# Kernel tuning notes

Hardware: AMD Instinct MI355X
Metric: run time of the kernel (lower is better)

The kernel has to match this reference:

```python
import jax, jax.numpy as jnp
import numpy as np


def _lstm_layer(x, W_ih, W_hh, b_ih, b_hh):
    # x: [B, T, D]; W_ih: [4H, D]; W_hh: [4H, H]; gate order (PyTorch): i, f, g, o
    B, T, _ = x.shape
    H = W_hh.shape[1]
    # Precompute input contributions for all timesteps: [B, T, 4H]
    xg = jnp.einsum('btd,gd->btg', x, W_ih) + b_ih + b_hh

    def step(carry, xg_t):
        h, c = carry
        gates = xg_t + h @ W_hh.T  # [B, 4H]
        i, f, g, o = jnp.split(gates, 4, axis=-1)
        i = jax.nn.sigmoid(i)
        f = jax.nn.sigmoid(f)
        g = jnp.tanh(g)
        o = jax.nn.sigmoid(o)
        c = f * c + i * g
        h = o * jnp.tanh(c)
        return (h, c), h

    h0 = jnp.zeros((B, H), dtype=x.dtype)
    c0 = jnp.zeros((B, H), dtype=x.dtype)
    (_, _), hs = jax.lax.scan(step, (h0, c0), jnp.swapaxes(xg, 0, 1))
    return jnp.swapaxes(hs, 0, 1)  # [B, T, H]


def setup_inputs() -> dict:
    key = jax.random.key(0)
    ks = jax.random.split(key, 11)
    B, T, D, H, C = 262144, 8, 8, 16, 10
    s = 1.0 / np.sqrt(H)  # PyTorch LSTM init scale
    return {
        'input_data': jax.random.normal(ks[0], (B, T, D), dtype=jnp.float32),
        'W_ih_l0': jax.random.uniform(ks[1], (4 * H, D), jnp.float32, -s, s),
        'W_hh_l0': jax.random.uniform(ks[2], (4 * H, H), jnp.float32, -s, s),
        'b_ih_l0': jax.random.uniform(ks[3], (4 * H,), jnp.float32, -s, s),
        'b_hh_l0': jax.random.uniform(ks[4], (4 * H,), jnp.float32, -s, s),
        'W_ih_l1': jax.random.uniform(ks[5], (4 * H, H), jnp.float32, -s, s),
        'W_hh_l1': jax.random.uniform(ks[6], (4 * H, H), jnp.float32, -s, s),
        'b_ih_l1': jax.random.uniform(ks[7], (4 * H,), jnp.float32, -s, s),
        'b_hh_l1': jax.random.uniform(ks[8], (4 * H,), jnp.float32, -s, s),
        'W_fc': jax.random.uniform(ks[9], (C, H), jnp.float32, -s, s),
        'b_fc': jax.random.uniform(ks[10], (C,), jnp.float32, -s, s),
    }


def reference(input_data, W_ih_l0, W_hh_l0, b_ih_l0, b_hh_l0,
              W_ih_l1, W_hh_l1, b_ih_l1, b_hh_l1, W_fc, b_fc):
    B = input_data.shape[0]
    x = input_data.reshape(B, 8, 8)
    h1 = _lstm_layer(x, W_ih_l0, W_hh_l0, b_ih_l0, b_hh_l0)   # [B, 8, 16]
    h2 = _lstm_layer(h1, W_ih_l1, W_hh_l1, b_ih_l1, b_hh_l1)  # [B, 8, 16]
    last = h2[:, -1, :]                                        # [B, 16]
    return last @ W_fc.T + b_fc                                # [B, 10]
```

## Files before the change

### kernel.cpp

```cpp
#include <hip/hip_runtime.h>

#define LOG2E 1.44269504088896340736f

typedef _Float16 f16x8  __attribute__((ext_vector_type(8)));
typedef float    f32x4  __attribute__((ext_vector_type(4)));

template <int I> struct IntC { static constexpr int value = I; };
template <int I, int N, typename F>
__device__ __forceinline__ void sfor(F&& f) {
    if constexpr (I < N) { f(IntC<I>{}); sfor<I + 1, N>(f); }
}

__device__ __forceinline__ float fexp2(float x){ return __builtin_amdgcn_exp2f(x); }
__device__ __forceinline__ float frcp(float x){ return __builtin_amdgcn_rcpf(x); }

__device__ __forceinline__ unsigned pkh(float a, float b){
    return __builtin_bit_cast(unsigned, __builtin_amdgcn_cvt_pkrtz(a, b));
}
__device__ __forceinline__ f16x8 mkBh(unsigned d0,unsigned d1,unsigned d2,unsigned d3){
    uint4 u{d0,d1,d2,d3};
    return __builtin_bit_cast(f16x8, u);
}

#define MFMA16H __builtin_amdgcn_mfma_f32_16x16x32_f16

__device__ __forceinline__ f32x4 cell_tail(const f32x4 (&dd)[4], f32x4& c){
    f32x4 Ei, Ef, Eg, Eo;
    sfor<0,4>([&](auto R){ constexpr int r=R.value;
        Ei[r] = fexp2(dd[0][r]);
        Ef[r] = fexp2(dd[1][r]);
        Eg[r] = fexp2(dd[2][r]);
        Eo[r] = fexp2(dd[3][r]);
    });
    f32x4 ov, cn;
    sfor<0,4>([&](auto R){ constexpr int r=R.value;
        float Ai = 1.f + Ei[r], Af = 1.f + Ef[r];
        float Ag = 1.f + Eg[r], Ao = 1.f + Eo[r];
        float L2 = Ai*Af, L3 = L2*Ag, P4 = L3*Ao;
        float S2 = Ag*Ao, S1 = Af*S2;
        float r4 = frcp(P4);
        float iv = S1*r4;
        float fv = (Ai*S2)*r4;
        float gr = (L2*Ao)*r4;
        ov[r]    = L3*r4;
        float gv = (Eg[r]-1.f)*gr;
        cn[r] = fv*c[r] + iv*gv;
    });
    c = cn;
    f32x4 tc;
    sfor<0,4>([&](auto R){ constexpr int r=R.value;
        tc[r] = fexp2(cn[r]*(2.f*LOG2E));
    });
    float B0=tc[0]+1.f, B1=tc[1]+1.f, B2=tc[2]+1.f, B3=tc[3]+1.f;
    float P2=B0*B1, P3=P2*B2, P4=P3*B3;
    float r4=frcp(P4);
    float R3=P3*r4;
    float r3=B3*r4;
    float R2=P2*r3;
    float r2=B2*r3;
    float R1=B0*r2;
    float R0=B1*r2;
    f32x4 hv;
    hv[0] = ov[0]*((tc[0]-1.f)*R0);
    hv[1] = ov[1]*((tc[1]-1.f)*R1);
    hv[2] = ov[2]*((tc[2]-1.f)*R2);
    hv[3] = ov[3]*((tc[3]-1.f)*R3);
    return hv;
}

__global__
__attribute__((amdgpu_flat_work_group_size(256,256)))
__attribute__((amdgpu_waves_per_eu(1,8)))
void lstm_mfma_kernel(const float* __restrict__ in,
                      const float* __restrict__ Wih0, const float* __restrict__ Whh0,
                      const float* __restrict__ bih0, const float* __restrict__ bhh0,
                      const float* __restrict__ Wih1, const float* __restrict__ Whh1,
                      const float* __restrict__ bih1, const float* __restrict__ bhh1,
                      const float* __restrict__ Wfc,  const float* __restrict__ bfc,
                      float* __restrict__ out, int B)
{
    const int lane = threadIdx.x & 63;
    const int wid  = threadIdx.x >> 6;
    const int q  = lane >> 4;
    const int sl = lane & 15;
    const long s0 = (long)(blockIdx.x*4 + wid)*64;

    f16x8 a0[4], a1[4];
    f32x4 bias0[4], bias1[4];
    sfor<0,4>([&](auto MT){ constexpr int mt = MT.value;
        constexpr float SC = (mt==2) ? (2.f*LOG2E) : (-LOG2E);
        const int gr = 16*mt + sl;
        sfor<0,8>([&](auto E){ constexpr int e = E.value;
            float w0;
            if constexpr (e < 4)      w0 = Whh0[gr*16 + 4*q + e];
            else if constexpr (e < 6) w0 = Wih0[gr*8 + 2*q + (e-4)];
            else                      w0 = 0.f;
            a0[mt][e] = (_Float16)(w0 * SC);
            float w1;
            if constexpr (e < 4) w1 = Wih1[gr*16 + 4*q + e];
            else                 w1 = Whh1[gr*16 + 4*q + (e-4)];
            a1[mt][e] = (_Float16)(w1 * SC);
        });
        sfor<0,4>([&](auto R){ constexpr int r = R.value;
            const int gb = 16*mt + 4*q + r;
            bias0[mt][r] = (bih0[gb] + bhh0[gb]) * SC;
            bias1[mt][r] = (bih1[gb] + bhh1[gb]) * SC;
        });
    });

    unsigned P0h[4]={0,0,0,0}, Q0h[4]={0,0,0,0};
    unsigned P1h[4]={0,0,0,0}, Q1h[4]={0,0,0,0};
    f32x4 c0[4], c1[4];
    sfor<0,4>([&](auto G){ constexpr int g=G.value;
        c0[g] = f32x4{0,0,0,0}; c1[g] = f32x4{0,0,0,0};
    });

    const float* xbase = in + (s0 + sl)*64 + 2*q;
    float2 xv[4];
    sfor<0,4>([&](auto G){ constexpr int g=G.value;
        xv[g] = *(const float2*)(xbase + g*1024);
    });

#pragma unroll 2
    for (int t = 0; t < 8; ++t) {
        const int nxt = (t==7) ? 0 : (t+1)*8;
        float2 xn[4];
        sfor<0,4>([&](auto G){ constexpr int g=G.value;
            xn[g] = *(const float2*)(xbase + g*1024 + nxt);
        });

        sfor<0,4>([&](auto G){ constexpr int g=G.value;
            const unsigned xh = pkh(xv[g].x, xv[g].y);
            f16x8 Bh = mkBh(P0h[g], Q0h[g], xh, 0u);
            f32x4 dd[4];
            sfor<0,4>([&](auto MT){ constexpr int mt = MT.value;
                dd[mt] = MFMA16H(a0[mt], Bh, bias0[mt], 0,0,0);
            });
            f32x4 hv = cell_tail(dd, c0[g]);
            P0h[g] = pkh(hv[0],hv[1]);  Q0h[g] = pkh(hv[2],hv[3]);
        });

        sfor<0,4>([&](auto G){ constexpr int g=G.value;
            f16x8 Bh = mkBh(P0h[g], Q0h[g], P1h[g], Q1h[g]);
            f32x4 dd[4];
            sfor<0,4>([&](auto MT){ constexpr int mt = MT.value;
                dd[mt] = MFMA16H(a1[mt], Bh, bias1[mt], 0,0,0);
            });
            f32x4 hv = cell_tail(dd, c1[g]);
            P1h[g] = pkh(hv[0],hv[1]);  Q1h[g] = pkh(hv[2],hv[3]);
        });

        sfor<0,4>([&](auto G){ constexpr int g=G.value; xv[g] = xn[g]; });
    }

    {
        f16x8 af;
        f32x4 biasf;
        sfor<0,8>([&](auto E){ constexpr int e = E.value;
            float wf = 0.f;
            if constexpr (e < 4) { if (sl < 10) wf = Wfc[sl*16 + 4*q + e]; }
            af[e] = (_Float16)wf;
        });
        sfor<0,4>([&](auto R){ constexpr int r = R.value;
            const int gb = 4*q + r;
            biasf[r] = (gb < 10) ? bfc[gb] : 0.f;
        });
        sfor<0,4>([&](auto G){ constexpr int g=G.value;
            f16x8 Bh = mkBh(P1h[g], Q1h[g], 0u, 0u);
            f32x4 d = MFMA16H(af, Bh, biasf, 0,0,0);
            float* orow = out + (s0 + g*16 + sl)*10;
            if (q == 0)      { *(float2*)(orow+0) = float2{d[0],d[1]}; *(float2*)(orow+2) = float2{d[2],d[3]}; }
            else if (q == 1) { *(float2*)(orow+4) = float2{d[0],d[1]}; *(float2*)(orow+6) = float2{d[2],d[3]}; }
            else if (q == 2) { *(float2*)(orow+8) = float2{d[0],d[1]}; }
        });
    }
}

extern "C" void kernel_launch(void* const* d_in, const int* in_sizes, int n_in,
                              void* d_out, int out_size, void* d_ws, size_t ws_size,
                              hipStream_t stream) {
    const float* in   = (const float*)d_in[0];
    const float* Wih0 = (const float*)d_in[1];
    const float* Whh0 = (const float*)d_in[2];
    const float* bih0 = (const float*)d_in[3];
    const float* bhh0 = (const float*)d_in[4];
    const float* Wih1 = (const float*)d_in[5];
    const float* Whh1 = (const float*)d_in[6];
    const float* bih1 = (const float*)d_in[7];
    const float* bhh1 = (const float*)d_in[8];
    const float* Wfc  = (const float*)d_in[9];
    const float* bfc  = (const float*)d_in[10];
    float* out = (float*)d_out;

    int B = in_sizes[0] / 64;
    int grid = B / 256;
    lstm_mfma_kernel<<<grid, 256, 0, stream>>>(in, Wih0, Whh0, bih0, bhh0,
                                               Wih1, Whh1, bih1, bhh1,
                                               Wfc, bfc, out, B);
}
```

Before: 89.04 us.

## Skew layer-0 and layer-1 timesteps and split sigmoid reciprocal

Restructures the recurrence into a software pipeline. Layer 0 runs one timestep ahead of layer 1 via a prologue and epilogue, so within each iteration the two layers' cells are independent and their MFMA and transcendental work can interleave. The gate math now uses two reciprocals over pairwise products instead of one reciprocal over a four-way product, which shortens the dependency chain at the cost of one extra rcp. Register pressure rises because the next layer-0 state is held alongside the current one.

```diff
diff --git a/kernel.cpp b/kernel.cpp
--- a/kernel.cpp
+++ b/kernel.cpp
@@ -36,13 +36,12 @@
     sfor<0,4>([&](auto R){ constexpr int r=R.value;
         float Ai = 1.f + Ei[r], Af = 1.f + Ef[r];
         float Ag = 1.f + Eg[r], Ao = 1.f + Eo[r];
-        float L2 = Ai*Af, L3 = L2*Ag, P4 = L3*Ao;
-        float S2 = Ag*Ao, S1 = Af*S2;
-        float r4 = frcp(P4);
-        float iv = S1*r4;
-        float fv = (Ai*S2)*r4;
-        float gr = (L2*Ao)*r4;
-        ov[r]    = L3*r4;
+        float p  = Ai*Af;  float rp = frcp(p);
+        float iv = Af*rp;
+        float fv = Ai*rp;
+        float q2 = Ag*Ao;  float rq = frcp(q2);
+        float gr = Ao*rq;
+        ov[r]    = Ag*rq;
         float gv = (Eg[r]-1.f)*gr;
         cn[r] = fv*c[r] + iv*gv;
     });
@@ -116,28 +115,37 @@
     });
 
     const float* xbase = in + (s0 + sl)*64 + 2*q;
+
     float2 xv[4];
     sfor<0,4>([&](auto G){ constexpr int g=G.value;
-        xv[g] = *(const float2*)(xbase + g*1024);
+        float2 x0 = *(const float2*)(xbase + g*1024);
+        xv[g]     = *(const float2*)(xbase + g*1024 + 8);
+        f16x8 Bh = mkBh(0u, 0u, pkh(x0.x, x0.y), 0u);
+        f32x4 dd[4];
+        sfor<0,4>([&](auto MT){ constexpr int mt = MT.value;
+            dd[mt] = MFMA16H(a0[mt], Bh, bias0[mt], 0,0,0);
+        });
+        f32x4 hv = cell_tail(dd, c0[g]);
+        P0h[g] = pkh(hv[0],hv[1]);  Q0h[g] = pkh(hv[2],hv[3]);
     });
 
 #pragma unroll 2
-    for (int t = 0; t < 8; ++t) {
-        const int nxt = (t==7) ? 0 : (t+1)*8;
+    for (int t = 0; t < 7; ++t) {
+        const int nxt = (t<=5) ? (t+2)*8 : 0;
         float2 xn[4];
         sfor<0,4>([&](auto G){ constexpr int g=G.value;
             xn[g] = *(const float2*)(xbase + g*1024 + nxt);
         });
 
-        sfor<0,4>([&](auto G){ constexpr int g=G.value;
-            const unsigned xh = pkh(xv[g].x, xv[g].y);
-            f16x8 Bh = mkBh(P0h[g], Q0h[g], xh, 0u);
+        unsigned nP0[4], nQ0[4];
+        sfor<0,4>([&](auto G){ constexpr int g=G.value;
+            f16x8 Bh = mkBh(P0h[g], Q0h[g], pkh(xv[g].x, xv[g].y), 0u);
             f32x4 dd[4];
             sfor<0,4>([&](auto MT){ constexpr int mt = MT.value;
                 dd[mt] = MFMA16H(a0[mt], Bh, bias0[mt], 0,0,0);
             });
             f32x4 hv = cell_tail(dd, c0[g]);
-            P0h[g] = pkh(hv[0],hv[1]);  Q0h[g] = pkh(hv[2],hv[3]);
+            nP0[g] = pkh(hv[0],hv[1]);  nQ0[g] = pkh(hv[2],hv[3]);
         });
 
         sfor<0,4>([&](auto G){ constexpr int g=G.value;
@@ -150,8 +158,20 @@
             P1h[g] = pkh(hv[0],hv[1]);  Q1h[g] = pkh(hv[2],hv[3]);
         });
 
-        sfor<0,4>([&](auto G){ constexpr int g=G.value; xv[g] = xn[g]; });
+        sfor<0,4>([&](auto G){ constexpr int g=G.value;
+            P0h[g] = nP0[g]; Q0h[g] = nQ0[g]; xv[g] = xn[g];
+        });
     }
+
+    sfor<0,4>([&](auto G){ constexpr int g=G.value;
+        f16x8 Bh = mkBh(P0h[g], Q0h[g], P1h[g], Q1h[g]);
+        f32x4 dd[4];
+        sfor<0,4>([&](auto MT){ constexpr int mt = MT.value;
+            dd[mt] = MFMA16H(a1[mt], Bh, bias1[mt], 0,0,0);
+        });
+        f32x4 hv = cell_tail(dd, c1[g]);
+        P1h[g] = pkh(hv[0],hv[1]);  Q1h[g] = pkh(hv[2],hv[3]);
+    });
 
     {
         f16x8 af;
```

New measurement: 92.70 us. 4.1% more time.
